# Optimization experiments

Measured on AMD Instinct MI355X. Metric: run time of the kernel, lower is better.

The kernel has to match this reference:

```python
import jax, jax.numpy as jnp
import numpy as np

N = 100000   # nodes
E = 1600000  # edges (avg degree 16)
DIN, DH, DOUT = 128, 128, 64


def setup_inputs() -> dict:
    key = jax.random.key(0)
    ks = jax.random.split(key, 6)
    feat = jax.random.normal(ks[0], (N, DIN), dtype=jnp.float32)
    src = jax.random.randint(ks[1], (E,), 0, N, dtype=jnp.int32)
    dst = jax.random.randint(ks[2], (E,), 0, N, dtype=jnp.int32)
    W0 = jax.random.normal(ks[3], (DIN, DH), dtype=jnp.float32) / np.sqrt(DIN)
    W1 = jax.random.normal(ks[4], (DH, DH), dtype=jnp.float32) / np.sqrt(DH)
    W2 = jax.random.normal(ks[5], (DH, DOUT), dtype=jnp.float32) / np.sqrt(DH)
    b0 = jnp.zeros((DH,), jnp.float32)
    b1 = jnp.zeros((DH,), jnp.float32)
    b2 = jnp.zeros((DOUT,), jnp.float32)
    return {"feat": feat, "W0": W0, "b0": b0, "W1": W1, "b1": b1,
            "W2": W2, "b2": b2, "src": src, "dst": dst}


def _gcn_layer(x, src, dst, W, b, n):
    # DGL GraphConv with norm='both': D_dst^{-1/2} A D_src^{-1/2} X W + b
    # (allow_zero_in_degree=True; degrees clamped to min 1 as in DGL)
    ones = jnp.ones((src.shape[0],), x.dtype)
    deg_out = jax.ops.segment_sum(ones, src, num_segments=n)
    deg_in = jax.ops.segment_sum(ones, dst, num_segments=n)
    norm_src = jnp.maximum(deg_out, 1.0) ** -0.5  # [N]
    norm_dst = jnp.maximum(deg_in, 1.0) ** -0.5   # [N]
    h = x * norm_src[:, None]                     # [N, d]
    agg = jax.ops.segment_sum(h[src], dst, num_segments=n)  # SpMM via gather+scatter
    h = agg * norm_dst[:, None]
    return h @ W + b


def reference(feat, W0, b0, W1, b1, W2, b2, src, dst):
    n = feat.shape[0]
    h = _gcn_layer(feat, src, dst, W0, b0, n)
    h = _gcn_layer(h, src, dst, W1, b1, n)
    h = _gcn_layer(h, src, dst, W2, b2, n)  # activation=None per defaults
    return h
```

## Files before the change

kernel.cpp:

```cpp
#include <hip/hip_runtime.h>
#include <hip/hip_fp16.h>


#define BIN_SHIFT 9
#define BIN_SIZE 512
#define NBINS_MAX 256
#define CAP 10240
#define P3_CHUNK 4096

typedef _Float16 f16x8 __attribute__((ext_vector_type(8)));
typedef float f32x4 __attribute__((ext_vector_type(4)));

__global__ __launch_bounds__(512) void p3_scatter(const int* __restrict__ src,
                                                  const int* __restrict__ dst,
                                                  int* __restrict__ bin_cur,
                                                  unsigned* __restrict__ binbuf,
                                                  unsigned short* __restrict__ srcbuf,
                                                  int E) {
    __shared__ int cd[NBINS_MAX];
    __shared__ int cs[NBINS_MAX];
    __shared__ int od[NBINS_MAX];
    __shared__ int osf[NBINS_MAX];
    const int tid = threadIdx.x;
    const int c0 = blockIdx.x * P3_CHUNK;
    const int c1 = min(E, c0 + P3_CHUNK);
    if (tid < NBINS_MAX) { cd[tid] = 0; cs[tid] = 0; }
    __syncthreads();
    for (int i = c0 + tid; i < c1; i += 512) {
        atomicAdd(&cd[dst[i] >> BIN_SHIFT], 1);
        atomicAdd(&cs[src[i] >> BIN_SHIFT], 1);
    }
    __syncthreads();
    if (tid < NBINS_MAX) {
        int d = cd[tid], s = cs[tid];
        if (d) od[tid] = atomicAdd(&bin_cur[tid], d);
        if (s) osf[tid] = atomicAdd(&bin_cur[NBINS_MAX + tid], s);
    }
    __syncthreads();
    if (tid < NBINS_MAX) { cd[tid] = 0; cs[tid] = 0; }
    __syncthreads();
    for (int i = c0 + tid; i < c1; i += 512) {
        int sv = src[i], dv = dst[i];
        int bd = dv >> BIN_SHIFT;
        int p = bd * CAP + od[bd] + atomicAdd(&cd[bd], 1);
        binbuf[p] = ((unsigned)sv << BIN_SHIFT) | (unsigned)(dv & (BIN_SIZE - 1));
        int bs = sv >> BIN_SHIFT;
        int q = bs * CAP + osf[bs] + atomicAdd(&cs[bs], 1);
        srcbuf[q] = (unsigned short)(sv & (BIN_SIZE - 1));
    }
}

__global__ __launch_bounds__(512) void p4_finalize(const unsigned* __restrict__ binbuf,
                                                   const int* __restrict__ bin_cur,
                                                   int* __restrict__ rp,
                                                   float* __restrict__ ndst,
                                                   int* __restrict__ eidx,
                                                   int n, int nbins) {
    __shared__ int hist[BIN_SIZE];
    __shared__ int wsum[8];
    __shared__ int s_base;
    const int tid = threadIdx.x;
    const int b = blockIdx.x;
    const int lane = tid & 63, w = tid >> 6;

    {
        int v = (tid < b) ? bin_cur[tid] : 0;
        int s = v;
#pragma unroll
        for (int off = 1; off < 64; off <<= 1) s += __shfl_xor(s, off, 64);
        if (lane == 0) wsum[w] = s;
    }
    hist[tid] = 0;
    __syncthreads();
    if (tid == 0) {
        int t = 0;
        for (int k = 0; k < 8; ++k) t += wsum[k];
        s_base = t;
    }
    __syncthreads();
    const int ebase = s_base;
    const int count = bin_cur[b];
    const unsigned* ebuf = binbuf + (size_t)b * CAP;

    for (int i = tid; i < count; i += 512)
        atomicAdd(&hist[ebuf[i] & (BIN_SIZE - 1)], 1);
    __syncthreads();

    const int hv = hist[tid];
    int sc = hv;
#pragma unroll
    for (int off = 1; off < 64; off <<= 1) {
        int t = __shfl_up(sc, off, 64);
        if (lane >= off) sc += t;
    }
    if (lane == 63) wsum[w] = sc;
    __syncthreads();
    int woff = 0;
    for (int k = 0; k < w; ++k) woff += wsum[k];
    const int excl = woff + sc - hv;

    const int g0 = (b << BIN_SHIFT) + tid;
    if (g0 < n) {
        rp[g0] = ebase + excl;
        ndst[g0] = rsqrtf(fmaxf((float)hv, 1.0f));
    }
    if (b == nbins - 1 && tid == 0) rp[n] = ebase + count;
    __syncthreads();
    hist[tid] = excl;
    __syncthreads();
    for (int i = tid; i < count; i += 512) {
        unsigned e = ebuf[i];
        int p = ebase + atomicAdd(&hist[e & (BIN_SIZE - 1)], 1);
        eidx[p] = (int)(e >> BIN_SHIFT);
    }
}

__global__ __launch_bounds__(512) void p4b_nsrc(const unsigned short* __restrict__ srcbuf,
                                                const int* __restrict__ bin_cur,
                                                const float* __restrict__ ndst,
                                                float* __restrict__ nsrc,
                                                float* __restrict__ nd2, int n) {
    __shared__ int hist[BIN_SIZE];
    const int tid = threadIdx.x;
    const int b = blockIdx.x;
    const int count = bin_cur[NBINS_MAX + b];
    hist[tid] = 0;
    __syncthreads();
    const unsigned short* ebuf = srcbuf + (size_t)b * CAP;
    for (int i = tid; i < count; i += 512)
        atomicAdd(&hist[ebuf[i]], 1);
    __syncthreads();
    const int g = (b << BIN_SHIFT) + tid;
    if (g < n) {
        float nv = rsqrtf(fmaxf((float)hist[tid], 1.0f));
        nsrc[g] = nv;
        nd2[g] = nv * ndst[g];
    }
}

__global__ __launch_bounds__(256) void wk1(const float* __restrict__ W0,
                                           const float* __restrict__ W1,
                                           const float* __restrict__ b0,
                                           float* __restrict__ T,
                                           float* __restrict__ v1) {
    int i = blockIdx.x * 256 + threadIdx.x;
    if (i < 16384) {
        int k = i >> 7, j = i & 127;
        float s = 0.f;
        for (int m = 0; m < 128; ++m) s += W0[k * 128 + m] * W1[m * 128 + j];
        T[i] = s;
    } else if (i < 16512) {
        int j = i - 16384;
        float s = 0.f;
        for (int m = 0; m < 128; ++m) s += b0[m] * W1[m * 128 + j];
        v1[j] = s;
    }
}

__global__ __launch_bounds__(256) void wk2(const float* __restrict__ T,
                                           const float* __restrict__ W2,
                                           const float* __restrict__ v1,
                                           const float* __restrict__ b1,
                                           _Float16* __restrict__ Wpt,
                                           float* __restrict__ c0,
                                           float* __restrict__ c1) {
    int i = blockIdx.x * 256 + threadIdx.x;
    if (i < 8192) {
        int k = i >> 6, c = i & 63;
        float s = 0.f;
        for (int j = 0; j < 128; ++j) s += T[k * 128 + j] * W2[j * 64 + c];
        Wpt[(size_t)c * 128 + k] = (_Float16)s;
    } else if (i < 8256) {
        int c = i - 8192;
        float s0 = 0.f, s1 = 0.f;
        for (int j = 0; j < 128; ++j) {
            s0 += v1[j] * W2[j * 64 + c];
            s1 += b1[j] * W2[j * 64 + c];
        }
        c0[c] = s0;
        c1[c] = s1;
    }
}

__global__ __launch_bounds__(256) void mfma_gemmG(const float* __restrict__ A,
                                                  const _Float16* __restrict__ Wpt,
                                                  const float* __restrict__ oscale,
                                                  _Float16* __restrict__ Y, int n) {
    const int wid = threadIdx.x >> 6;
    const int lane = threadIdx.x & 63;
    const int row0 = (blockIdx.x * 4 + wid) * 16;
    if (row0 >= n) return;
    const int lr = lane & 15;
    const int hi = lane >> 4;
    const int lk = hi * 8;

    const float* arow = A + (size_t)(row0 + lr) * 128 + lk;
    f16x8 a[4];
#pragma unroll
    for (int s = 0; s < 4; ++s) {
        float4 p0 = *(const float4*)(arow + s * 32);
        float4 p1 = *(const float4*)(arow + s * 32 + 4);
        f16x8 h;
        h[0] = (_Float16)p0.x; h[1] = (_Float16)p0.y;
        h[2] = (_Float16)p0.z; h[3] = (_Float16)p0.w;
        h[4] = (_Float16)p1.x; h[5] = (_Float16)p1.y;
        h[6] = (_Float16)p1.z; h[7] = (_Float16)p1.w;
        a[s] = h;
    }

    const int rbase = row0 + hi * 4;
    float os[4];
#pragma unroll
    for (int j = 0; j < 4; ++j) os[j] = oscale[rbase + j];

#pragma unroll
    for (int ct = 0; ct < 4; ++ct) {
        const int col = ct * 16 + lr;
        const _Float16* wrow = Wpt + (size_t)col * 128 + lk;
        f32x4 acc = {0.f, 0.f, 0.f, 0.f};
#pragma unroll
        for (int s = 0; s < 4; ++s) {
            f16x8 b = *(const f16x8*)(wrow + s * 32);
            acc = __builtin_amdgcn_mfma_f32_16x16x32_f16(a[s], b, acc, 0, 0, 0);
        }
#pragma unroll
        for (int j = 0; j < 4; ++j)
            Y[(size_t)(rbase + j) * 64 + col] = (_Float16)(acc[j] * os[j]);
    }
}

template <int MODE>
__global__ __launch_bounds__(256) void gather_mid(const _Float16* __restrict__ x,
                                                  const int* __restrict__ eidx,
                                                  const int* __restrict__ rp,
                                                  const float* __restrict__ nd2,
                                                  const float* __restrict__ ndst,
                                                  const float* __restrict__ svec,
                                                  const float* __restrict__ nsrc,
                                                  _Float16* __restrict__ out,
                                                  float* __restrict__ sout,
                                                  float* __restrict__ sout2, int n) {
    const int node = blockIdx.x * 32 + (threadIdx.x >> 3);
    const int lane = threadIdx.x & 7;
    if (node >= n) return;
    const int beg = rp[node], end = rp[node + 1];
    float acc[8] = {0.f, 0.f, 0.f, 0.f, 0.f, 0.f, 0.f, 0.f};
    float sv = 0.f;
#pragma unroll 2
    for (int e = beg; e < end; ++e) {
        int s = eidx[e];
        f16x8 v = *(const f16x8*)(x + (size_t)s * 64 + lane * 8);
#pragma unroll
        for (int j = 0; j < 8; ++j) acc[j] += (float)v[j];
        if (lane == 0) sv += svec[s];
    }
    const float sd = nd2[node];
    f16x8 r;
#pragma unroll
    for (int j = 0; j < 8; ++j) r[j] = (_Float16)(acc[j] * sd);
    __builtin_nontemporal_store(r, (f16x8*)(out + (size_t)node * 64 + lane * 8));
    if (lane == 0) {
        float t = ndst[node] * sv;
        if (MODE == 1) {
            sout[node] = t;
            sout2[node] = nsrc[node] * t;
        } else {
            sout[node] = t;
        }
    }
}

__global__ __launch_bounds__(256) void gather_final(const _Float16* __restrict__ x,
                                                    const int* __restrict__ eidx,
                                                    const int* __restrict__ rp,
                                                    const float* __restrict__ ndst,
                                                    const float* __restrict__ u,
                                                    const float* __restrict__ w,
                                                    const float* __restrict__ c0,
                                                    const float* __restrict__ c1,
                                                    const float* __restrict__ b2,
                                                    float* __restrict__ out, int n) {
    const int node = blockIdx.x * 32 + (threadIdx.x >> 3);
    const int lane = threadIdx.x & 7;
    if (node >= n) return;
    const int beg = rp[node], end = rp[node + 1];
    float acc[8] = {0.f, 0.f, 0.f, 0.f, 0.f, 0.f, 0.f, 0.f};
#pragma unroll 2
    for (int e = beg; e < end; ++e) {
        int s = eidx[e];
        f16x8 v = *(const f16x8*)(x + (size_t)s * 64 + lane * 8);
#pragma unroll
        for (int j = 0; j < 8; ++j) acc[j] += (float)v[j];
    }
    const float sd = ndst[node];
    const float ui = u[node];
    const float wi = w[node];
    const float4* C0 = (const float4*)(c0 + lane * 8);
    const float4* C1 = (const float4*)(c1 + lane * 8);
    const float4* B2 = (const float4*)(b2 + lane * 8);
    float4 c0a = C0[0], c0b = C0[1];
    float4 c1a = C1[0], c1b = C1[1];
    float4 b2a = B2[0], b2b = B2[1];
    float* o = out + (size_t)node * 64 + lane * 8;
    ((float4*)o)[0] = make_float4(acc[0] * sd + wi * c0a.x + ui * c1a.x + b2a.x,
                                  acc[1] * sd + wi * c0a.y + ui * c1a.y + b2a.y,
                                  acc[2] * sd + wi * c0a.z + ui * c1a.z + b2a.z,
                                  acc[3] * sd + wi * c0a.w + ui * c1a.w + b2a.w);
    ((float4*)o)[1] = make_float4(acc[4] * sd + wi * c0b.x + ui * c1b.x + b2b.x,
                                  acc[5] * sd + wi * c0b.y + ui * c1b.y + b2b.y,
                                  acc[6] * sd + wi * c0b.z + ui * c1b.z + b2b.z,
                                  acc[7] * sd + wi * c0b.w + ui * c1b.w + b2b.w);
}

static inline int cdiv(long long a, long long b) { return (int)((a + b - 1) / b); }

extern "C" void kernel_launch(void* const* d_in, const int* in_sizes, int n_in,
                              void* d_out, int out_size, void* d_ws, size_t ws_size,
                              hipStream_t stream) {
    const float* feat = (const float*)d_in[0];
    const float* W0   = (const float*)d_in[1];
    const float* b0   = (const float*)d_in[2];
    const float* W1   = (const float*)d_in[3];
    const float* b1   = (const float*)d_in[4];
    const float* W2   = (const float*)d_in[5];
    const float* b2   = (const float*)d_in[6];
    const int*   src  = (const int*)d_in[7];
    const int*   dst  = (const int*)d_in[8];

    const int N = in_sizes[0] / 128;
    const int E = in_sizes[7];

    float* ws       = (float*)d_ws;
    float* nsrc     = ws;
    float* ndst     = ws + (size_t)N;
    float* nd2      = ws + 2 * (size_t)N;
    float* u        = ws + 3 * (size_t)N;
    float* su       = ws + 4 * (size_t)N;
    float* w        = ws + 5 * (size_t)N;
    int*   rp       = (int*)(ws + 6 * (size_t)N);
    int*   bin_cur  = rp + (N + 1);
    int*   eidx     = bin_cur + 2 * NBINS_MAX;
    float* T        = (float*)(eidx + E);
    float* v1       = T + 16384;
    float* c0       = v1 + 128;
    float* c1       = c0 + 64;
    size_t aoff     = (size_t)(7 * (size_t)N + 1 + 2 * NBINS_MAX + E + 16640 + 15) & ~(size_t)15;
    _Float16* bufA  = (_Float16*)(ws + aoff);
    _Float16* bufB  = (_Float16*)(ws + aoff + (size_t)N * 32);
    _Float16* Wpt   = (_Float16*)(ws + aoff + (size_t)N * 64);
    unsigned* binbuf       = (unsigned*)bufA;
    unsigned short* srcbuf = (unsigned short*)bufB;

    const int NBINS_USED = cdiv(N, BIN_SIZE);

    hipMemsetAsync(bin_cur, 0, 2 * NBINS_MAX * sizeof(int), stream);
    p3_scatter<<<cdiv(E, P3_CHUNK), 512, 0, stream>>>(src, dst, bin_cur, binbuf, srcbuf, E);
    p4_finalize<<<NBINS_USED, 512, 0, stream>>>(binbuf, bin_cur, rp, ndst, eidx, N, NBINS_USED);
    p4b_nsrc<<<NBINS_USED, 512, 0, stream>>>(srcbuf, bin_cur, ndst, nsrc, nd2, N);

    wk1<<<65, 256, 0, stream>>>(W0, W1, b0, T, v1);
    wk2<<<33, 256, 0, stream>>>(T, W2, v1, b1, Wpt, c0, c1);

    mfma_gemmG<<<cdiv(N, 64), 256, 0, stream>>>(feat, Wpt, nsrc, bufA, N);

    const int gblocks = cdiv(N, 32);
    gather_mid<1><<<gblocks, 256, 0, stream>>>(bufA, eidx, rp, nd2, ndst, nsrc, nsrc,
                                               bufB, u, su, N);
    gather_mid<2><<<gblocks, 256, 0, stream>>>(bufB, eidx, rp, nd2, ndst, su, nullptr,
                                               bufA, w, nullptr, N);
    gather_final<<<gblocks, 256, 0, stream>>>(bufA, eidx, rp, ndst, u, w, c0, c1, b2,
                                              (float*)d_out, N);
}
```

Baseline: 270.8 us.

## Fuse source-degree histogram into finalize and reassociate weight products

Merges the separate source-degree kernel into p4_finalize, so both degree histograms are built in one launch and nsrc/nd2 are written together. The weight prefold now computes W1·W2 (128x64) first and then W0·U, instead of the 128x128 W0·W1 product, which cuts the FLOPs and the intermediate size. The gather kernel spreads the per-edge scalar svec accumulation across 8 lanes and combines them with shuffles, instead of serialising it on lane 0. The cost is one more shared histogram per block and more work inside p4_finalize.

```diff
diff --git a/kernel.cpp b/kernel.cpp
--- a/kernel.cpp
+++ b/kernel.cpp
@@ -51,12 +51,16 @@
 }
 
 __global__ __launch_bounds__(512) void p4_finalize(const unsigned* __restrict__ binbuf,
+                                                   const unsigned short* __restrict__ srcbuf,
                                                    const int* __restrict__ bin_cur,
                                                    int* __restrict__ rp,
                                                    float* __restrict__ ndst,
+                                                   float* __restrict__ nsrc,
+                                                   float* __restrict__ nd2,
                                                    int* __restrict__ eidx,
                                                    int n, int nbins) {
     __shared__ int hist[BIN_SIZE];
+    __shared__ int hist2[BIN_SIZE];
     __shared__ int wsum[8];
     __shared__ int s_base;
     const int tid = threadIdx.x;
@@ -71,6 +75,7 @@
         if (lane == 0) wsum[w] = s;
     }
     hist[tid] = 0;
+    hist2[tid] = 0;
     __syncthreads();
     if (tid == 0) {
         int t = 0;
@@ -80,10 +85,14 @@
     __syncthreads();
     const int ebase = s_base;
     const int count = bin_cur[b];
+    const int scount = bin_cur[NBINS_MAX + b];
     const unsigned* ebuf = binbuf + (size_t)b * CAP;
+    const unsigned short* sbuf = srcbuf + (size_t)b * CAP;
 
     for (int i = tid; i < count; i += 512)
         atomicAdd(&hist[ebuf[i] & (BIN_SIZE - 1)], 1);
+    for (int i = tid; i < scount; i += 512)
+        atomicAdd(&hist2[sbuf[i]], 1);
     __syncthreads();
 
     const int hv = hist[tid];
@@ -102,7 +111,11 @@
     const int g0 = (b << BIN_SHIFT) + tid;
     if (g0 < n) {
         rp[g0] = ebase + excl;
-        ndst[g0] = rsqrtf(fmaxf((float)hv, 1.0f));
+        float nd = rsqrtf(fmaxf((float)hv, 1.0f));
+        float nv = rsqrtf(fmaxf((float)hist2[tid], 1.0f));
+        ndst[g0] = nd;
+        nsrc[g0] = nv;
+        nd2[g0] = nv * nd;
     }
     if (b == nbins - 1 && tid == 0) rp[n] = ebase + count;
     __syncthreads();
@@ -115,70 +128,41 @@
     }
 }
 
-__global__ __launch_bounds__(512) void p4b_nsrc(const unsigned short* __restrict__ srcbuf,
-                                                const int* __restrict__ bin_cur,
-                                                const float* __restrict__ ndst,
-                                                float* __restrict__ nsrc,
-                                                float* __restrict__ nd2, int n) {
-    __shared__ int hist[BIN_SIZE];
-    const int tid = threadIdx.x;
-    const int b = blockIdx.x;
-    const int count = bin_cur[NBINS_MAX + b];
-    hist[tid] = 0;
-    __syncthreads();
-    const unsigned short* ebuf = srcbuf + (size_t)b * CAP;
-    for (int i = tid; i < count; i += 512)
-        atomicAdd(&hist[ebuf[i]], 1);
-    __syncthreads();
-    const int g = (b << BIN_SHIFT) + tid;
-    if (g < n) {
-        float nv = rsqrtf(fmaxf((float)hist[tid], 1.0f));
-        nsrc[g] = nv;
-        nd2[g] = nv * ndst[g];
-    }
-}
-
-__global__ __launch_bounds__(256) void wk1(const float* __restrict__ W0,
-                                           const float* __restrict__ W1,
-                                           const float* __restrict__ b0,
-                                           float* __restrict__ T,
-                                           float* __restrict__ v1) {
-    int i = blockIdx.x * 256 + threadIdx.x;
-    if (i < 16384) {
-        int k = i >> 7, j = i & 127;
-        float s = 0.f;
-        for (int m = 0; m < 128; ++m) s += W0[k * 128 + m] * W1[m * 128 + j];
-        T[i] = s;
-    } else if (i < 16512) {
-        int j = i - 16384;
-        float s = 0.f;
-        for (int m = 0; m < 128; ++m) s += b0[m] * W1[m * 128 + j];
-        v1[j] = s;
-    }
-}
-
-__global__ __launch_bounds__(256) void wk2(const float* __restrict__ T,
+__global__ __launch_bounds__(256) void wk1(const float* __restrict__ W1,
                                            const float* __restrict__ W2,
-                                           const float* __restrict__ v1,
                                            const float* __restrict__ b1,
-                                           _Float16* __restrict__ Wpt,
-                                           float* __restrict__ c0,
+                                           float* __restrict__ U,
                                            float* __restrict__ c1) {
     int i = blockIdx.x * 256 + threadIdx.x;
     if (i < 8192) {
         int k = i >> 6, c = i & 63;
         float s = 0.f;
-        for (int j = 0; j < 128; ++j) s += T[k * 128 + j] * W2[j * 64 + c];
+        for (int j = 0; j < 128; ++j) s += W1[k * 128 + j] * W2[j * 64 + c];
+        U[i] = s;
+    } else if (i < 8256) {
+        int c = i - 8192;
+        float s = 0.f;
+        for (int j = 0; j < 128; ++j) s += b1[j] * W2[j * 64 + c];
+        c1[c] = s;
+    }
+}
+
+__global__ __launch_bounds__(256) void wk2(const float* __restrict__ W0,
+                                           const float* __restrict__ U,
+                                           const float* __restrict__ b0,
+                                           _Float16* __restrict__ Wpt,
+                                           float* __restrict__ c0) {
+    int i = blockIdx.x * 256 + threadIdx.x;
+    if (i < 8192) {
+        int k = i >> 6, c = i & 63;
+        float s = 0.f;
+        for (int j = 0; j < 128; ++j) s += W0[k * 128 + j] * U[j * 64 + c];
         Wpt[(size_t)c * 128 + k] = (_Float16)s;
     } else if (i < 8256) {
         int c = i - 8192;
-        float s0 = 0.f, s1 = 0.f;
-        for (int j = 0; j < 128; ++j) {
-            s0 += v1[j] * W2[j * 64 + c];
-            s1 += b1[j] * W2[j * 64 + c];
-        }
-        c0[c] = s0;
-        c1[c] = s1;
+        float s = 0.f;
+        for (int j = 0; j < 128; ++j) s += b0[j] * U[j * 64 + c];
+        c0[c] = s;
     }
 }
 
@@ -252,13 +236,16 @@
         f16x8 v = *(const f16x8*)(x + (size_t)s * 64 + lane * 8);
 #pragma unroll
         for (int j = 0; j < 8; ++j) acc[j] += (float)v[j];
-        if (lane == 0) sv += svec[s];
+        if (((e - beg) & 7) == lane) sv += svec[s];
     }
     const float sd = nd2[node];
     f16x8 r;
 #pragma unroll
     for (int j = 0; j < 8; ++j) r[j] = (_Float16)(acc[j] * sd);
     __builtin_nontemporal_store(r, (f16x8*)(out + (size_t)node * 64 + lane * 8));
+    sv += __shfl_xor(sv, 1, 8);
+    sv += __shfl_xor(sv, 2, 8);
+    sv += __shfl_xor(sv, 4, 8);
     if (lane == 0) {
         float t = ndst[node] * sv;
         if (MODE == 1) {
@@ -340,11 +327,10 @@
     int*   rp       = (int*)(ws + 6 * (size_t)N);
     int*   bin_cur  = rp + (N + 1);
     int*   eidx     = bin_cur + 2 * NBINS_MAX;
-    float* T        = (float*)(eidx + E);
-    float* v1       = T + 16384;
-    float* c0       = v1 + 128;
+    float* U        = (float*)(eidx + E);
+    float* c0       = U + 8192;
     float* c1       = c0 + 64;
-    size_t aoff     = (size_t)(7 * (size_t)N + 1 + 2 * NBINS_MAX + E + 16640 + 15) & ~(size_t)15;
+    size_t aoff     = (size_t)(7 * (size_t)N + 1 + 2 * NBINS_MAX + E + 8320 + 15) & ~(size_t)15;
     _Float16* bufA  = (_Float16*)(ws + aoff);
     _Float16* bufB  = (_Float16*)(ws + aoff + (size_t)N * 32);
     _Float16* Wpt   = (_Float16*)(ws + aoff + (size_t)N * 64);
@@ -355,11 +341,11 @@
 
     hipMemsetAsync(bin_cur, 0, 2 * NBINS_MAX * sizeof(int), stream);
     p3_scatter<<<cdiv(E, P3_CHUNK), 512, 0, stream>>>(src, dst, bin_cur, binbuf, srcbuf, E);
-    p4_finalize<<<NBINS_USED, 512, 0, stream>>>(binbuf, bin_cur, rp, ndst, eidx, N, NBINS_USED);
-    p4b_nsrc<<<NBINS_USED, 512, 0, stream>>>(srcbuf, bin_cur, ndst, nsrc, nd2, N);
-
-    wk1<<<65, 256, 0, stream>>>(W0, W1, b0, T, v1);
-    wk2<<<33, 256, 0, stream>>>(T, W2, v1, b1, Wpt, c0, c1);
+    p4_finalize<<<NBINS_USED, 512, 0, stream>>>(binbuf, srcbuf, bin_cur, rp, ndst,
+                                                nsrc, nd2, eidx, N, NBINS_USED);
+
+    wk1<<<33, 256, 0, stream>>>(W1, W2, b1, U, c1);
+    wk2<<<33, 256, 0, stream>>>(W0, U, b0, Wpt, c0);
 
     mfma_gemmG<<<cdiv(N, 64), 256, 0, stream>>>(feat, Wpt, nsrc, bufA, N);
 
```

After: 268.5 us. Within noise of the previous version (-0.9%).
